# Optimization experiments

Measured on AMD Instinct MI355X. Metric: run time of the kernel, lower is better.

The kernel has to match this reference:

```python
import jax, jax.numpy as jnp
import numpy as np

B, S, D, H = 2, 2048, 1024, 16
DK = D // H


def setup_inputs() -> dict:
    key = jax.random.key(0)
    ks = jax.random.split(key, 11)
    inp = {
        'query': jax.random.normal(ks[0], (B, S, D), jnp.float32),
        'key':   jax.random.normal(ks[1], (B, S, D), jnp.float32),
        'value': jax.random.normal(ks[2], (B, S, D), jnp.float32),
        # causal mask, broadcast over heads like mask.unsqueeze(1)
        'mask': jnp.broadcast_to(jnp.tril(jnp.ones((S, S), jnp.int32)), (B, S, S)),
    }
    s = 1.0 / np.sqrt(D)
    for i, nm in enumerate(['q', 'k', 'v', 'o']):
        inp[f'W{nm}'] = jax.random.normal(ks[3 + i], (D, D), jnp.float32) * s
        inp[f'b{nm}'] = jnp.zeros((D,), jnp.float32)
    return inp


def reference(query, key, value, mask, Wq, bq, Wk, bk, Wv, bv, Wo, bo):
    def proj(x, W, b):
        # [B,S,D] -> [B,H,S,DK]
        y = x @ W.T + b
        return y.reshape(B, S, H, DK).transpose(0, 2, 1, 3)

    q = proj(query, Wq, bq)
    k = proj(key, Wk, bk)
    v = proj(value, Wv, bv)

    scores = jnp.einsum('bhsd,bhtd->bhst', q, k) / np.sqrt(DK)
    scores = jnp.where(mask[:, None, :, :] == 0, -1e9, scores)
    p = jax.nn.softmax(scores, axis=-1)  # dropout in eval mode = identity
    x = jnp.einsum('bhst,bhtd->bhsd', p, v)
    x = x.transpose(0, 2, 1, 3).reshape(B, S, D)
    return x @ Wo.T + bo
```

## Files before the change

kernel.cpp:

```cpp
#include <hip/hip_runtime.h>
#include <stdint.h>

#define BB 2
#define SS 2048
#define DD 1024
#define HH 16
#define DKK 64
#define EE 4194304
#define WEE 1048576
#define QSCALE 0.1803368801f

typedef __attribute__((ext_vector_type(8))) short bf16x8;
typedef __attribute__((ext_vector_type(4))) float f32x4;
typedef __attribute__((ext_vector_type(4))) unsigned short u16x4;

__device__ __forceinline__ unsigned short f2bf(float f) {
    union { float f; unsigned int i; } c; c.f = f;
    unsigned int u = c.i;
    return (unsigned short)((u + 0x7FFFu + ((u >> 16) & 1u)) >> 16);
}
__device__ __forceinline__ float bf2f(unsigned short u) {
    union { float f; unsigned int i; } c; c.i = ((unsigned int)u) << 16; return c.f;
}
__device__ __forceinline__ float load1f(const void* p, int idx, int isbf) {
    return isbf ? bf2f(((const unsigned short*)p)[idx]) : ((const float*)p)[idx];
}

#define GLDS16(gp, lp)                                                              \
    __builtin_amdgcn_global_load_lds(                                               \
        (const __attribute__((address_space(1))) void*)(gp),                        \
        (__attribute__((address_space(3))) void*)(lp), 16, 0, 0)

__global__ void detect_dtype_k(const unsigned short* __restrict__ q,
                               int* __restrict__ flag) {
    const int lane = threadIdx.x;
    unsigned short u = q[lane * 2];
    int ex = (u >> 7) & 0xFF;
    bool bad = (ex != 0) && (ex < 110 || ex > 137);
    unsigned long long m = __ballot(bad);
    if (lane == 0) *flag = (__popcll(m) >= 8) ? 0 : 1;
}

__global__ __launch_bounds__(256)
void convert_k(const float* __restrict__ q, const float* __restrict__ k,
               const float* __restrict__ v,
               const float* __restrict__ wq, const float* __restrict__ wk,
               const float* __restrict__ wv, const float* __restrict__ wo,
               unsigned short* __restrict__ Xc, unsigned short* __restrict__ Wc,
               const int* __restrict__ flagp)
{
    if (*flagp) return;
    const size_t e = ((size_t)blockIdx.x * 256 + threadIdx.x) * 8;
    const float* src; unsigned short* dst; size_t off;
    if (e < (size_t)3 * EE) {
        const int t = (int)(e / EE);
        src = (t == 0) ? q : (t == 1) ? k : v;
        off = e - (size_t)t * EE;
        dst = Xc + (size_t)t * EE;
    } else {
        const size_t we = e - (size_t)3 * EE;
        const int t = (int)(we >> 20);
        src = (t == 0) ? wq : (t == 1) ? wk : (t == 2) ? wv : wo;
        off = we & (WEE - 1);
        dst = Wc + (size_t)t * WEE;
    }
    const float4 a = *(const float4*)(src + off);
    const float4 b = *(const float4*)(src + off + 4);
    bf16x8 o;
    o[0] = (short)f2bf(a.x); o[1] = (short)f2bf(a.y);
    o[2] = (short)f2bf(a.z); o[3] = (short)f2bf(a.w);
    o[4] = (short)f2bf(b.x); o[5] = (short)f2bf(b.y);
    o[6] = (short)f2bf(b.z); o[7] = (short)f2bf(b.w);
    *(bf16x8*)(dst + off) = o;
}

__global__ __launch_bounds__(256)
void gemm_qkv(const void* __restrict__ Xq, const void* __restrict__ Xk,
              const void* __restrict__ Xv,
              const void* __restrict__ Wqp, const void* __restrict__ Wkp,
              const void* __restrict__ Wvp,
              const void* __restrict__ bqp, const void* __restrict__ bkp,
              const void* __restrict__ bvp,
              const unsigned short* __restrict__ Xc,
              const unsigned short* __restrict__ Wc,
              unsigned short* __restrict__ qb, unsigned short* __restrict__ kb,
              unsigned short* __restrict__ vtb, const int* __restrict__ flagp)
{
    const int isbf = *flagp;
    const int z = blockIdx.z;
    const unsigned short* Xg = isbf
        ? (const unsigned short*)((z == 0) ? Xq : (z == 1) ? Xk : Xv)
        : Xc + (size_t)z * EE;
    const unsigned short* Wg = isbf
        ? (const unsigned short*)((z == 0) ? Wqp : (z == 1) ? Wkp : Wvp)
        : Wc + (size_t)z * WEE;
    const void* bias = (z == 0) ? bqp : (z == 1) ? bkp : bvp;

    __shared__ __align__(16) unsigned short As[3][128 * 32];
    __shared__ __align__(16) unsigned short Bs[3][128 * 32];

    const int tid  = threadIdx.x;
    const int lane = tid & 63, w = tid >> 6;
    const int l15  = lane & 15, quad = lane >> 4;
    const int wr = (w >> 1) * 64, wc = (w & 1) * 64;
    const int r0 = blockIdx.x * 128, c0 = blockIdx.y * 128;
    const int srow = tid >> 2;
    const int scol = (((tid & 3) ^ ((tid >> 3) & 3)) << 3);
    const int rdo  = ((quad ^ ((l15 >> 1) & 3)) << 3);

    const unsigned short* xp0 = Xg + (size_t)(r0 + srow) * DD + scol;
    const unsigned short* xp1 = Xg + (size_t)(r0 + 64 + srow) * DD + scol;
    const unsigned short* wp0 = Wg + (size_t)(c0 + srow) * DD + scol;
    const unsigned short* wp1 = Wg + (size_t)(c0 + 64 + srow) * DD + scol;

#define STAGE_G(buf, kk)                                                       \
    do {                                                                       \
        GLDS16(xp0 + (kk), &As[buf][tid * 8]);                                 \
        GLDS16(xp1 + (kk), &As[buf][2048 + tid * 8]);                          \
        GLDS16(wp0 + (kk), &Bs[buf][tid * 8]);                                 \
        GLDS16(wp1 + (kk), &Bs[buf][2048 + tid * 8]);                          \
    } while (0)

#define COMPUTE_G(buf)                                                         \
    do {                                                                       \
        bf16x8 af[4], bfr[4];                                                  \
        _Pragma("unroll")                                                      \
        for (int mi = 0; mi < 4; ++mi)                                         \
            af[mi] = *(const bf16x8*)(&As[buf][(wr + mi * 16 + l15) * 32 +     \
                                               rdo]);                          \
        _Pragma("unroll")                                                      \
        for (int ni = 0; ni < 4; ++ni)                                         \
            bfr[ni] = *(const bf16x8*)(&Bs[buf][(wc + ni * 16 + l15) * 32 +    \
                                                rdo]);                         \
        _Pragma("unroll")                                                      \
        for (int mi = 0; mi < 4; ++mi)                                         \
            _Pragma("unroll")                                                  \
            for (int ni = 0; ni < 4; ++ni)                                     \
                acc[mi][ni] = __builtin_amdgcn_mfma_f32_16x16x32_bf16(         \
                    af[mi], bfr[ni], acc[mi][ni], 0, 0, 0);                    \
    } while (0)

#define PHASE_G(cb, nb, kn)                                                    \
    do {                                                                       \
        asm volatile("s_waitcnt vmcnt(4)" ::: "memory");                       \
        __builtin_amdgcn_s_barrier();                                          \
        __builtin_amdgcn_sched_barrier(0);                                     \
        STAGE_G(nb, kn);                                                       \
        __builtin_amdgcn_sched_barrier(0);                                     \
        COMPUTE_G(cb);                                                         \
    } while (0)

    f32x4 acc[4][4] = {};

    STAGE_G(0, 0);
    STAGE_G(1, 32);
    for (int s = 0; s < 30; s += 3) {
        const int k0 = s * 32;
        PHASE_G(0, 2, k0 + 64);
        PHASE_G(1, 0, k0 + 96);
        PHASE_G(2, 1, k0 + 128);
    }
    asm volatile("s_waitcnt vmcnt(4)" ::: "memory");
    __builtin_amdgcn_s_barrier();
    __builtin_amdgcn_sched_barrier(0);
    COMPUTE_G(0);
    asm volatile("s_waitcnt vmcnt(0)" ::: "memory");
    __builtin_amdgcn_s_barrier();
    __builtin_amdgcn_sched_barrier(0);
    COMPUTE_G(1);

#pragma unroll
    for (int mi = 0; mi < 4; ++mi) {
#pragma unroll
        for (int ni = 0; ni < 4; ++ni) {
            const int col = c0 + wc + ni * 16 + l15;
            const float bv = load1f(bias, col, isbf);
            const int h = col >> 6, dk = col & 63;
            const int m0 = r0 + wr + mi * 16 + quad * 4;
            const int bb = m0 >> 11, s0 = m0 & (SS - 1);
            const int bh = bb * HH + h;
            if (z == 0) {
#pragma unroll
                for (int r = 0; r < 4; ++r)
                    qb[((size_t)bh * SS + s0 + r) * DKK + dk] =
                        f2bf((acc[mi][ni][r] + bv) * QSCALE);
            } else if (z == 1) {
#pragma unroll
                for (int r = 0; r < 4; ++r) {
                    const int t = s0 + r;
                    kb[((((size_t)bh * 128 + (t >> 4)) * 8 + (dk >> 3)) * 16 +
                        (t & 15)) * 8 + (dk & 7)] = f2bf(acc[mi][ni][r] + bv);
                }
            } else {
                u16x4 pv;
#pragma unroll
                for (int r = 0; r < 4; ++r) pv[r] = f2bf(acc[mi][ni][r] + bv);
                const int t = s0;
                *(u16x4*)&vtb[((((size_t)bh * 64 + (t >> 5)) * 4 + (dk >> 4)) * 64 +
                               ((t >> 3) & 3) * 16 + (dk & 15)) * 8 + (t & 7)] = pv;
            }
        }
    }
#undef STAGE_G
#undef COMPUTE_G
#undef PHASE_G
}

template <bool MASKED>
__device__ __forceinline__ void attn_tile(
    const int t0, const int q0, const int l15, const int quad,
    const unsigned short* __restrict__ Kb, const unsigned short* __restrict__ Vb,
    const bf16x8 (&qf)[2], f32x4 (&Oa)[4], float (&ls)[4],
    unsigned short* __restrict__ Pw)
{
    bf16x8 kf[4][2];
#pragma unroll
    for (int ni = 0; ni < 4; ++ni)
#pragma unroll
        for (int ks = 0; ks < 2; ++ks)
            kf[ni][ks] = *(const bf16x8*)(Kb +
                ((size_t)(((t0 >> 4) + ni) * 8 + ks * 4 + quad) * 16 + l15) * 8);

    f32x4 sc[4] = {};
#pragma unroll
    for (int ks = 0; ks < 2; ++ks)
#pragma unroll
        for (int ni = 0; ni < 4; ++ni)
            sc[ni] = __builtin_amdgcn_mfma_f32_16x16x32_bf16(
                qf[ks], kf[ni][ks], sc[ni], 0, 0, 0);

    bf16x8 vf[4][2];
#pragma unroll
    for (int nd = 0; nd < 4; ++nd)
#pragma unroll
        for (int ks = 0; ks < 2; ++ks)
            vf[nd][ks] = *(const bf16x8*)(Vb +
                ((size_t)(((t0 >> 5) + ks) * 4 + nd) * 64 + quad * 16 + l15) * 8);

#pragma unroll
    for (int ni = 0; ni < 4; ++ni)
#pragma unroll
        for (int r = 0; r < 4; ++r) {
            float s = sc[ni][r];
            if (MASKED && (t0 + ni * 16 + l15 > q0 + quad * 4 + r))
                s = -__builtin_inff();
            const float p = exp2f(s);
            const unsigned int pu = __float_as_uint(p);
            ls[r] += __uint_as_float(pu & 0xFFFF0000u);
            Pw[(quad * 4 + r) * 72 + ni * 16 + l15] = (unsigned short)(pu >> 16);
        }

    bf16x8 pf[2];
#pragma unroll
    for (int ks = 0; ks < 2; ++ks)
        pf[ks] = *(const bf16x8*)(Pw + l15 * 72 + ks * 32 + quad * 8);
#pragma unroll
    for (int ks = 0; ks < 2; ++ks)
#pragma unroll
        for (int nd = 0; nd < 4; ++nd)
            Oa[nd] = __builtin_amdgcn_mfma_f32_16x16x32_bf16(
                pf[ks], vf[nd][ks], Oa[nd], 0, 0, 0);
}

__global__ __launch_bounds__(256)
void attn_mfma(const unsigned short* __restrict__ Qg,
               const unsigned short* __restrict__ Kf,
               const unsigned short* __restrict__ Vf,
               unsigned short* __restrict__ Og)
{
    __shared__ __align__(16) unsigned short Ps[4][16 * 72];
    const int tid  = threadIdx.x;
    const int lane = tid & 63, w = tid >> 6;
    const int l15 = lane & 15, quad = lane >> 4;
    const int bh = blockIdx.x;
    const int qt = (gridDim.y - 1 - blockIdx.y) * 4 + w;
    const int q0 = qt * 16;
    unsigned short* Pw = &Ps[w][0];

    const unsigned short* Qb = Qg + (size_t)bh * SS * DKK;
    const unsigned short* Kb = Kf + (size_t)bh * SS * DKK;
    const unsigned short* Vb = Vf + (size_t)bh * SS * DKK;

    bf16x8 qf[2];
#pragma unroll
    for (int ks = 0; ks < 2; ++ks)
        qf[ks] = *(const bf16x8*)(Qb + (size_t)(q0 + l15) * DKK + ks * 32 + quad * 8);

    f32x4 Oa[4] = {};
    float ls[4] = {};
    const int nfull = q0 >> 6;

    for (int tt = 0; tt < nfull; ++tt)
        attn_tile<false>(tt * 64, q0, l15, quad, Kb, Vb, qf, Oa, ls, Pw);
    attn_tile<true>(nfull * 64, q0, l15, quad, Kb, Vb, qf, Oa, ls, Pw);

    const int bb = bh >> 4, h = bh & (HH - 1);
#pragma unroll
    for (int r = 0; r < 4; ++r) {
        float l = ls[r];
        l += __shfl_xor(l, 1);
        l += __shfl_xor(l, 2);
        l += __shfl_xor(l, 4);
        l += __shfl_xor(l, 8);
        const float inv = 1.0f / l;
        const int s = q0 + quad * 4 + r;
#pragma unroll
        for (int nd = 0; nd < 4; ++nd)
            Og[((size_t)bb * SS + s) * DD + h * 64 + nd * 16 + l15] =
                f2bf(Oa[nd][r] * inv);
    }
}

__global__ __launch_bounds__(256)
void gemm_out(const unsigned short* __restrict__ Xa, const void* __restrict__ W,
              const unsigned short* __restrict__ Wcs,
              const void* __restrict__ bias, void* __restrict__ Y,
              const int* __restrict__ flagp)
{
    const int isbf = *flagp;
    const unsigned short* Wg = isbf ? (const unsigned short*)W : Wcs;

    __shared__ __align__(16) unsigned short As[3][128 * 32];
    __shared__ __align__(16) unsigned short Bs[3][128 * 32];

    const int tid  = threadIdx.x;
    const int lane = tid & 63, w = tid >> 6;
    const int l15  = lane & 15, quad = lane >> 4;
    const int wr = (w >> 1) * 64, wc = (w & 1) * 64;
    const int r0 = blockIdx.x * 128, c0 = blockIdx.y * 128;
    const int srow = tid >> 2;
    const int scol = (((tid & 3) ^ ((tid >> 3) & 3)) << 3);
    const int rdo  = ((quad ^ ((l15 >> 1) & 3)) << 3);

    const unsigned short* xp0 = Xa + (size_t)(r0 + srow) * DD + scol;
    const unsigned short* xp1 = Xa + (size_t)(r0 + 64 + srow) * DD + scol;
    const unsigned short* wp0 = Wg + (size_t)(c0 + srow) * DD + scol;
    const unsigned short* wp1 = Wg + (size_t)(c0 + 64 + srow) * DD + scol;

#define STAGE_O(buf, kk)                                                       \
    do {                                                                       \
        GLDS16(xp0 + (kk), &As[buf][tid * 8]);                                 \
        GLDS16(xp1 + (kk), &As[buf][2048 + tid * 8]);                          \
        GLDS16(wp0 + (kk), &Bs[buf][tid * 8]);                                 \
        GLDS16(wp1 + (kk), &Bs[buf][2048 + tid * 8]);                          \
    } while (0)

#define COMPUTE_O(buf)                                                         \
    do {                                                                       \
        bf16x8 af[4], bfr[4];                                                  \
        _Pragma("unroll")                                                      \
        for (int mi = 0; mi < 4; ++mi)                                         \
            af[mi] = *(const bf16x8*)(&As[buf][(wr + mi * 16 + l15) * 32 +     \
                                               rdo]);                          \
        _Pragma("unroll")                                                      \
        for (int ni = 0; ni < 4; ++ni)                                         \
            bfr[ni] = *(const bf16x8*)(&Bs[buf][(wc + ni * 16 + l15) * 32 +    \
                                                rdo]);                         \
        _Pragma("unroll")                                                      \
        for (int mi = 0; mi < 4; ++mi)                                         \
            _Pragma("unroll")                                                  \
            for (int ni = 0; ni < 4; ++ni)                                     \
                acc[mi][ni] = __builtin_amdgcn_mfma_f32_16x16x32_bf16(         \
                    af[mi], bfr[ni], acc[mi][ni], 0, 0, 0);                    \
    } while (0)

#define PHASE_O(cb, nb, kn)                                                    \
    do {                                                                       \
        asm volatile("s_waitcnt vmcnt(4)" ::: "memory");                       \
        __builtin_amdgcn_s_barrier();                                          \
        __builtin_amdgcn_sched_barrier(0);                                     \
        STAGE_O(nb, kn);                                                       \
        __builtin_amdgcn_sched_barrier(0);                                     \
        COMPUTE_O(cb);                                                         \
    } while (0)

    f32x4 acc[4][4] = {};

    STAGE_O(0, 0);
    STAGE_O(1, 32);
    for (int s = 0; s < 30; s += 3) {
        const int k0 = s * 32;
        PHASE_O(0, 2, k0 + 64);
        PHASE_O(1, 0, k0 + 96);
        PHASE_O(2, 1, k0 + 128);
    }
    asm volatile("s_waitcnt vmcnt(4)" ::: "memory");
    __builtin_amdgcn_s_barrier();
    __builtin_amdgcn_sched_barrier(0);
    COMPUTE_O(0);
    asm volatile("s_waitcnt vmcnt(0)" ::: "memory");
    __builtin_amdgcn_s_barrier();
    __builtin_amdgcn_sched_barrier(0);
    COMPUTE_O(1);

#pragma unroll
    for (int mi = 0; mi < 4; ++mi) {
#pragma unroll
        for (int ni = 0; ni < 4; ++ni) {
            const int col = c0 + wc + ni * 16 + l15;
            const float bv = load1f(bias, col, isbf);
            const int m0 = r0 + wr + mi * 16 + quad * 4;
#pragma unroll
            for (int r = 0; r < 4; ++r) {
                const float val = acc[mi][ni][r] + bv;
                if (isbf) ((unsigned short*)Y)[(size_t)(m0 + r) * DD + col] = f2bf(val);
                else      ((float*)Y)[(size_t)(m0 + r) * DD + col] = val;
            }
        }
    }
#undef STAGE_O
#undef COMPUTE_O
#undef PHASE_O
}

extern "C" void kernel_launch(void* const* d_in, const int* in_sizes, int n_in,
                              void* d_out, int out_size, void* d_ws, size_t ws_size,
                              hipStream_t stream)
{
    const void* query = d_in[0];
    const void* key   = d_in[1];
    const void* value = d_in[2];
    const void* Wq = d_in[4];  const void* bq = d_in[5];
    const void* Wk = d_in[6];  const void* bk = d_in[7];
    const void* Wv = d_in[8];  const void* bv = d_in[9];
    const void* Wo = d_in[10]; const void* bo = d_in[11];

    int* flag = (int*)d_ws;
    unsigned short* base = (unsigned short*)((char*)d_ws + 256);
    const size_t E = EE;
    unsigned short* qb  = base;
    unsigned short* kb  = base + E;
    unsigned short* vtb = base + 2 * E;
    unsigned short* Wc  = base + 3 * E;
    unsigned short* Xc  = base + 4 * E;
    unsigned short* ab  = Xc;

    detect_dtype_k<<<1, 64, 0, stream>>>((const unsigned short*)query, flag);
    convert_k<<<8192, 256, 0, stream>>>((const float*)query, (const float*)key,
                                        (const float*)value, (const float*)Wq,
                                        (const float*)Wk, (const float*)Wv,
                                        (const float*)Wo, Xc, Wc, flag);
    gemm_qkv<<<dim3(32, 8, 3), 256, 0, stream>>>(query, key, value, Wq, Wk, Wv,
                                                 bq, bk, bv, Xc, Wc,
                                                 qb, kb, vtb, flag);
    attn_mfma<<<dim3(32, 32), 256, 0, stream>>>(qb, kb, vtb, ab);
    gemm_out<<<dim3(32, 8), 256, 0, stream>>>(ab, Wo, Wc + 3 * (size_t)WEE, bo,
                                              d_out, flag);
}
```

Before: 249.4 us.

## Shrink output GEMM tiles, hoist LDS fragment loads, add MFMA priority hints

The output projection GEMM now uses 64x128 tiles instead of 128x128, doubling its grid to 512 blocks so more of the 256 CUs get work. The A-tile staging and the waitcnt are adjusted to match. In both GEMMs the LDS fragment reads now happen before the next global-to-LDS stage is issued, and the MFMA blocks are wrapped in s_setprio raises. The attention MFMAs get the same priority hints. The trade-off is less data reuse per block in the output GEMM and possible register-pressure or scheduling changes.

```diff
diff --git a/kernel.cpp b/kernel.cpp
--- a/kernel.cpp
+++ b/kernel.cpp
@@ -121,9 +121,8 @@
         GLDS16(wp1 + (kk), &Bs[buf][2048 + tid * 8]);                          \
     } while (0)
 
-#define COMPUTE_G(buf)                                                         \
-    do {                                                                       \
-        bf16x8 af[4], bfr[4];                                                  \
+#define LOADFRAG_G(buf)                                                        \
+    do {                                                                       \
         _Pragma("unroll")                                                      \
         for (int mi = 0; mi < 4; ++mi)                                         \
             af[mi] = *(const bf16x8*)(&As[buf][(wr + mi * 16 + l15) * 32 +     \
@@ -132,12 +131,18 @@
         for (int ni = 0; ni < 4; ++ni)                                         \
             bfr[ni] = *(const bf16x8*)(&Bs[buf][(wc + ni * 16 + l15) * 32 +    \
                                                 rdo]);                         \
+    } while (0)
+
+#define MFMA_G()                                                               \
+    do {                                                                       \
+        __builtin_amdgcn_s_setprio(1);                                         \
         _Pragma("unroll")                                                      \
         for (int mi = 0; mi < 4; ++mi)                                         \
             _Pragma("unroll")                                                  \
             for (int ni = 0; ni < 4; ++ni)                                     \
                 acc[mi][ni] = __builtin_amdgcn_mfma_f32_16x16x32_bf16(         \
                     af[mi], bfr[ni], acc[mi][ni], 0, 0, 0);                    \
+        __builtin_amdgcn_s_setprio(0);                                         \
     } while (0)
 
 #define PHASE_G(cb, nb, kn)                                                    \
@@ -145,12 +150,14 @@
         asm volatile("s_waitcnt vmcnt(4)" ::: "memory");                       \
         __builtin_amdgcn_s_barrier();                                          \
         __builtin_amdgcn_sched_barrier(0);                                     \
+        LOADFRAG_G(cb);                                                        \
         STAGE_G(nb, kn);                                                       \
         __builtin_amdgcn_sched_barrier(0);                                     \
-        COMPUTE_G(cb);                                                         \
+        MFMA_G();                                                              \
     } while (0)
 
     f32x4 acc[4][4] = {};
+    bf16x8 af[4], bfr[4];
 
     STAGE_G(0, 0);
     STAGE_G(1, 32);
@@ -163,11 +170,13 @@
     asm volatile("s_waitcnt vmcnt(4)" ::: "memory");
     __builtin_amdgcn_s_barrier();
     __builtin_amdgcn_sched_barrier(0);
-    COMPUTE_G(0);
+    LOADFRAG_G(0);
+    MFMA_G();
     asm volatile("s_waitcnt vmcnt(0)" ::: "memory");
     __builtin_amdgcn_s_barrier();
     __builtin_amdgcn_sched_barrier(0);
-    COMPUTE_G(1);
+    LOADFRAG_G(1);
+    MFMA_G();
 
 #pragma unroll
     for (int mi = 0; mi < 4; ++mi) {
@@ -202,7 +211,8 @@
         }
     }
 #undef STAGE_G
-#undef COMPUTE_G
+#undef LOADFRAG_G
+#undef MFMA_G
 #undef PHASE_G
 }
 
@@ -222,12 +232,14 @@
                 ((size_t)(((t0 >> 4) + ni) * 8 + ks * 4 + quad) * 16 + l15) * 8);
 
     f32x4 sc[4] = {};
+    __builtin_amdgcn_s_setprio(1);
 #pragma unroll
     for (int ks = 0; ks < 2; ++ks)
 #pragma unroll
         for (int ni = 0; ni < 4; ++ni)
             sc[ni] = __builtin_amdgcn_mfma_f32_16x16x32_bf16(
                 qf[ks], kf[ni][ks], sc[ni], 0, 0, 0);
+    __builtin_amdgcn_s_setprio(0);
 
     bf16x8 vf[4][2];
 #pragma unroll
@@ -254,12 +266,14 @@
 #pragma unroll
     for (int ks = 0; ks < 2; ++ks)
         pf[ks] = *(const bf16x8*)(Pw + l15 * 72 + ks * 32 + quad * 8);
+    __builtin_amdgcn_s_setprio(1);
 #pragma unroll
     for (int ks = 0; ks < 2; ++ks)
 #pragma unroll
         for (int nd = 0; nd < 4; ++nd)
             Oa[nd] = __builtin_amdgcn_mfma_f32_16x16x32_bf16(
                 pf[ks], vf[nd][ks], Oa[nd], 0, 0, 0);
+    __builtin_amdgcn_s_setprio(0);
 }
 
 __global__ __launch_bounds__(256)
@@ -320,61 +334,66 @@
     const int isbf = *flagp;
     const unsigned short* Wg = isbf ? (const unsigned short*)W : Wcs;
 
-    __shared__ __align__(16) unsigned short As[3][128 * 32];
+    __shared__ __align__(16) unsigned short As[3][64 * 32];
     __shared__ __align__(16) unsigned short Bs[3][128 * 32];
 
     const int tid  = threadIdx.x;
     const int lane = tid & 63, w = tid >> 6;
     const int l15  = lane & 15, quad = lane >> 4;
-    const int wr = (w >> 1) * 64, wc = (w & 1) * 64;
-    const int r0 = blockIdx.x * 128, c0 = blockIdx.y * 128;
+    const int wr = (w >> 1) * 32, wc = (w & 1) * 64;
+    const int r0 = blockIdx.x * 64, c0 = blockIdx.y * 128;
     const int srow = tid >> 2;
     const int scol = (((tid & 3) ^ ((tid >> 3) & 3)) << 3);
     const int rdo  = ((quad ^ ((l15 >> 1) & 3)) << 3);
 
     const unsigned short* xp0 = Xa + (size_t)(r0 + srow) * DD + scol;
-    const unsigned short* xp1 = Xa + (size_t)(r0 + 64 + srow) * DD + scol;
     const unsigned short* wp0 = Wg + (size_t)(c0 + srow) * DD + scol;
     const unsigned short* wp1 = Wg + (size_t)(c0 + 64 + srow) * DD + scol;
 
 #define STAGE_O(buf, kk)                                                       \
     do {                                                                       \
         GLDS16(xp0 + (kk), &As[buf][tid * 8]);                                 \
-        GLDS16(xp1 + (kk), &As[buf][2048 + tid * 8]);                          \
         GLDS16(wp0 + (kk), &Bs[buf][tid * 8]);                                 \
         GLDS16(wp1 + (kk), &Bs[buf][2048 + tid * 8]);                          \
     } while (0)
 
-#define COMPUTE_O(buf)                                                         \
-    do {                                                                       \
-        bf16x8 af[4], bfr[4];                                                  \
-        _Pragma("unroll")                                                      \
-        for (int mi = 0; mi < 4; ++mi)                                         \
+#define LOADFRAG_O(buf)                                                        \
+    do {                                                                       \
+        _Pragma("unroll")                                                      \
+        for (int mi = 0; mi < 2; ++mi)                                         \
             af[mi] = *(const bf16x8*)(&As[buf][(wr + mi * 16 + l15) * 32 +     \
                                                rdo]);                          \
         _Pragma("unroll")                                                      \
         for (int ni = 0; ni < 4; ++ni)                                         \
             bfr[ni] = *(const bf16x8*)(&Bs[buf][(wc + ni * 16 + l15) * 32 +    \
                                                 rdo]);                         \
-        _Pragma("unroll")                                                      \
-        for (int mi = 0; mi < 4; ++mi)                                         \
+    } while (0)
+
+#define MFMA_O()                                                               \
+    do {                                                                       \
+        __builtin_amdgcn_s_setprio(1);                                         \
+        _Pragma("unroll")                                                      \
+        for (int mi = 0; mi < 2; ++mi)                                         \
             _Pragma("unroll")                                                  \
             for (int ni = 0; ni < 4; ++ni)                                     \
                 acc[mi][ni] = __builtin_amdgcn_mfma_f32_16x16x32_bf16(         \
                     af[mi], bfr[ni], acc[mi][ni], 0, 0, 0);                    \
+        __builtin_amdgcn_s_setprio(0);                                         \
     } while (0)
 
 #define PHASE_O(cb, nb, kn)                                                    \
     do {                                                                       \
-        asm volatile("s_waitcnt vmcnt(4)" ::: "memory");                       \
+        asm volatile("s_waitcnt vmcnt(3)" ::: "memory");                       \
         __builtin_amdgcn_s_barrier();                                          \
         __builtin_amdgcn_sched_barrier(0);                                     \
+        LOADFRAG_O(cb);                                                        \
         STAGE_O(nb, kn);                                                       \
         __builtin_amdgcn_sched_barrier(0);                                     \
-        COMPUTE_O(cb);                                                         \
-    } while (0)
-
-    f32x4 acc[4][4] = {};
+        MFMA_O();                                                              \
+    } while (0)
+
+    f32x4 acc[2][4] = {};
+    bf16x8 af[2], bfr[4];
 
     STAGE_O(0, 0);
     STAGE_O(1, 32);
@@ -384,17 +403,19 @@
         PHASE_O(1, 0, k0 + 96);
         PHASE_O(2, 1, k0 + 128);
     }
-    asm volatile("s_waitcnt vmcnt(4)" ::: "memory");
+    asm volatile("s_waitcnt vmcnt(3)" ::: "memory");
     __builtin_amdgcn_s_barrier();
     __builtin_amdgcn_sched_barrier(0);
-    COMPUTE_O(0);
+    LOADFRAG_O(0);
+    MFMA_O();
     asm volatile("s_waitcnt vmcnt(0)" ::: "memory");
     __builtin_amdgcn_s_barrier();
     __builtin_amdgcn_sched_barrier(0);
-    COMPUTE_O(1);
-
-#pragma unroll
-    for (int mi = 0; mi < 4; ++mi) {
+    LOADFRAG_O(1);
+    MFMA_O();
+
+#pragma unroll
+    for (int mi = 0; mi < 2; ++mi) {
 #pragma unroll
         for (int ni = 0; ni < 4; ++ni) {
             const int col = c0 + wc + ni * 16 + l15;
@@ -409,7 +430,8 @@
         }
     }
 #undef STAGE_O
-#undef COMPUTE_O
+#undef LOADFRAG_O
+#undef MFMA_O
 #undef PHASE_O
 }
 
@@ -444,6 +466,6 @@
                                                  bq, bk, bv, Xc, Wc,
                                                  qb, kb, vtb, flag);
     attn_mfma<<<dim3(32, 32), 256, 0, stream>>>(qb, kb, vtb, ab);
-    gemm_out<<<dim3(32, 8), 256, 0, stream>>>(ab, Wo, Wc + 3 * (size_t)WEE, bo,
+    gemm_out<<<dim3(64, 8), 256, 0, stream>>>(ab, Wo, Wc + 3 * (size_t)WEE, bo,
                                               d_out, flag);
 }
```

Measured after the change: 233.4 us. 6.4% less time.
